# Kernel optimization log

Measured on AMD Instinct MI355X. Metric: run time of the kernel, lower is better.

Reference implementation:

```python
import jax, jax.numpy as jnp
import numpy as np

HIDDEN = 512
DETER = 1024
STOCH = 32
OBS = 1024
ACT = 64
B, T = 64, 256


def _linear_params(key, out_dim, in_dim):
    kw, kb = jax.random.split(key)
    scale = 1.0 / np.sqrt(in_dim)
    W = jax.random.uniform(kw, (out_dim, in_dim), jnp.float32, -scale, scale)
    b = jax.random.uniform(kb, (out_dim,), jnp.float32, -scale, scale)
    return W, b


def setup_inputs() -> dict:
    key = jax.random.key(0)
    ks = jax.random.split(key, 12)
    obs_embeds = jax.random.normal(ks[0], (B, T, OBS), jnp.float32)
    action_embs = jax.random.normal(ks[1], (B, T, ACT), jnp.float32)
    noise_prior = jax.random.normal(ks[2], (B, T, STOCH), jnp.float32)
    noise_post = jax.random.normal(ks[3], (B, T, STOCH), jnp.float32)
    W_sa, b_sa = _linear_params(ks[4], DETER, STOCH + ACT)
    W_ih, b_ih = _linear_params(ks[5], 3 * DETER, DETER)
    W_hh, b_hh = _linear_params(ks[6], 3 * DETER, DETER)
    Wp1, bp1 = _linear_params(ks[7], HIDDEN, DETER)
    Wp2, bp2 = _linear_params(ks[8], 2 * STOCH, HIDDEN)
    Wq1, bq1 = _linear_params(ks[9], HIDDEN, DETER + OBS)
    Wq2, bq2 = _linear_params(ks[10], 2 * STOCH, HIDDEN)
    return {
        "obs_embeds": obs_embeds, "action_embs": action_embs,
        "noise_prior": noise_prior, "noise_post": noise_post,
        "W_sa": W_sa, "b_sa": b_sa,
        "W_ih": W_ih, "b_ih": b_ih, "W_hh": W_hh, "b_hh": b_hh,
        "Wp1": Wp1, "bp1": bp1, "Wp2": Wp2, "bp2": bp2,
        "Wq1": Wq1, "bq1": bq1, "Wq2": Wq2, "bq2": bq2,
    }


def _rollout(obs_embeds, action_embs, noise_prior, noise_post,
             W_sa, b_sa, W_ih, b_ih, W_hh, b_hh,
             Wp1, bp1, Wp2, bp2, Wq1, bq1, Wq2, bq2):
    S = Wp2.shape[0] // 2
    eps = 1e-5

    def gru(x, h):  # torch GRUCell: gates ordered r, z, n
        gi = x @ W_ih.T + b_ih
        gh = h @ W_hh.T + b_hh
        ir, iz, inn = jnp.split(gi, 3, axis=-1)
        hr, hz, hn = jnp.split(gh, 3, axis=-1)
        r = jax.nn.sigmoid(ir + hr)
        z = jax.nn.sigmoid(iz + hz)
        n = jnp.tanh(inn + r * hn)
        return (1.0 - z) * n + z * h

    def step(carry, inp):
        deter, stoch = carry
        obs, act, n_p, n_q = inp
        # prior: h_t = f(s_{t-1}, a_{t-1}, h_{t-1})
        emb = jax.nn.relu(jnp.concatenate([stoch, act], -1) @ W_sa.T + b_sa)
        deter = gru(emb, deter)
        pm_s = jax.nn.relu(deter @ Wp1.T + bp1) @ Wp2.T + bp2
        p_mean = pm_s[..., :S]
        p_std = jax.nn.softplus(pm_s[..., S:]) + eps
        p_stoch = p_mean + p_std * n_p
        # posterior: p(s_t | h_t, o_t)
        qm_s = jax.nn.relu(jnp.concatenate([deter, obs], -1) @ Wq1.T + bq1) @ Wq2.T + bq2
        q_mean = qm_s[..., :S]
        q_std = jax.nn.softplus(qm_s[..., S:]) + eps
        q_stoch = q_mean + q_std * n_q
        out = jnp.concatenate([deter, p_mean, p_std, p_stoch, q_mean, q_std, q_stoch], -1)
        return (deter, q_stoch), out

    batch = obs_embeds.shape[0]
    deter0 = jnp.zeros((batch, W_hh.shape[1]), obs_embeds.dtype)
    stoch0 = jnp.zeros((batch, S), obs_embeds.dtype)
    xs = (
        jnp.swapaxes(obs_embeds, 0, 1),
        jnp.swapaxes(action_embs, 0, 1),
        jnp.swapaxes(noise_prior, 0, 1),
        jnp.swapaxes(noise_post, 0, 1),
    )
    _, outs = jax.lax.scan(step, (deter0, stoch0), xs)
    return jnp.swapaxes(outs, 0, 1)  # [B, T, deter + 6*stoch]


def reference(obs_embeds, action_embs, noise_prior, noise_post,
              W_sa, b_sa, W_ih, b_ih, W_hh, b_hh,
              Wp1, bp1, Wp2, bp2, Wq1, bq1, Wq2, bq2):
    return _rollout(obs_embeds, action_embs, noise_prior, noise_post,
                    W_sa, b_sa, W_ih, b_ih, W_hh, b_hh,
                    Wp1, bp1, Wp2, bp2, Wq1, bq1, Wq2, bq2)
```

## Files before the change

kernel.cpp:

```cpp
#include <hip/hip_runtime.h>
#include <math.h>

#define B_   64
#define T_   256
#define OUTD 1216

typedef unsigned short ushort_t;
typedef unsigned int   uint32;
typedef __attribute__((ext_vector_type(8))) short bfrag;
typedef __attribute__((ext_vector_type(4))) float f32x4;
typedef __attribute__((ext_vector_type(4))) unsigned short us4;

__device__ __forceinline__ float sigmoidf_(float x) { return 1.0f / (1.0f + __expf(-x)); }
__device__ __forceinline__ float softplusf_(float x) { return (x > 20.0f) ? x : log1pf(__expf(x)); }
__device__ __forceinline__ ushort_t f2bf(float f) {
    uint32 u = __float_as_uint(f);
    u += 0x7fffu + ((u >> 16) & 1u);
    return (ushort_t)(u >> 16);
}
__device__ __forceinline__ float bf2f(ushort_t u) { return __uint_as_float(((uint32)u) << 16); }

__global__ void kwprep(const float* __restrict__ Wih, const float* __restrict__ Whh,
                       const float* __restrict__ Wp1, const float* __restrict__ Wq1,
                       const float* __restrict__ Wp2, const float* __restrict__ Wq2,
                       const float* __restrict__ Wsa,
                       ushort_t* Wih_b, ushort_t* Whh_b, ushort_t* Wp1_b, ushort_t* Wq1_b,
                       ushort_t* W2sw, ushort_t* Wsasw) {
    int stride = gridDim.x * blockDim.x;
    int gid = blockIdx.x * blockDim.x + threadIdx.x;
    for (int i = gid; i < 3072 * 1024; i += stride) Wih_b[i] = f2bf(Wih[i]);
    for (int i = gid; i < 3072 * 1024; i += stride) Whh_b[i] = f2bf(Whh[i]);
    for (int i = gid; i < 512 * 1024; i += stride) Wp1_b[i] = f2bf(Wp1[i]);
    for (int i = gid; i < 512 * 2048; i += stride) Wq1_b[i] = f2bf(Wq1[i]);
    for (int i = gid; i < 65536; i += stride) {
        int head = i >> 15, g = (i >> 9) & 63, o = (i >> 3) & 63, ii = i & 7;
        const float* src = head ? Wq2 : Wp2;
        W2sw[i] = f2bf(src[o * 512 + g * 8 + ii]);
    }
    for (int i = gid; i < 98304; i += stride) {
        int g = i >> 13, j = (i >> 3) & 1023, ii = i & 7;
        Wsasw[i] = f2bf(Wsa[j * 96 + g * 8 + ii]);
    }
}

__global__ void kinit(const float* __restrict__ act, const float* __restrict__ Wsa,
                      const float* __restrict__ bsa,
                      ushort_t* emb_sw, ushort_t* det_sw0, float* det_fp0) {
    int gid = blockIdx.x * 256 + threadIdx.x;
    int j = gid >> 6, b = gid & 63;
    float acc = bsa[j];
    const float* a = act + (size_t)b * T_ * 64;
    const float* w = Wsa + j * 96 + 32;
#pragma unroll 8
    for (int c = 0; c < 64; ++c) acc += a[c] * w[c];
    emb_sw[((j >> 3) * 64 + b) * 8 + (j & 7)] = f2bf(fmaxf(acc, 0.f));
    det_sw0[gid] = 0;
    det_fp0[gid] = 0.f;
}

__global__ __launch_bounds__(256) void kgru(int t,
        const ushort_t* __restrict__ Wih, const ushort_t* __restrict__ Whh,
        const float* __restrict__ bih, const float* __restrict__ bhh,
        const ushort_t* __restrict__ emb_sw, const ushort_t* __restrict__ det_sw_in,
        const float* __restrict__ det_fp_in,
        ushort_t* __restrict__ det_sw_out, float* __restrict__ det_fp_out,
        const float* __restrict__ obs, ushort_t* __restrict__ obs_sw,
        float* __restrict__ out) {
    if (blockIdx.x >= 64) {
        int kb = (blockIdx.x - 64) * 64;
        int tx = threadIdx.x & 63, ty = threadIdx.x >> 6;
        for (int b = ty; b < 64; b += 4) {
            int k = kb + tx;
            float v = obs[((size_t)b * T_ + t) * 1024 + k];
            obs_sw[((k >> 3) * 64 + b) * 8 + (k & 7)] = f2bf(v);
        }
        return;
    }
    __shared__ float red[2 * 24 * 256];
    const int tid = threadIdx.x;
    const int lane = tid & 63, w = tid >> 6;
    const int m = lane & 15, quad = lane >> 4;
    const int j0 = blockIdx.x * 16;

    f32x4 acc[2][3][4];
#pragma unroll
    for (int a2 = 0; a2 < 2; ++a2)
#pragma unroll
        for (int g = 0; g < 3; ++g)
#pragma unroll
            for (int n = 0; n < 4; ++n) acc[a2][g][n] = (f32x4){0.f, 0.f, 0.f, 0.f};

    const int kb0 = w * 256;
    const ushort_t* arow[2][3];
#pragma unroll
    for (int g = 0; g < 3; ++g) {
        arow[0][g] = Wih + (size_t)(g * 1024 + j0 + m) * 1024 + kb0 + quad * 8;
        arow[1][g] = Whh + (size_t)(g * 1024 + j0 + m) * 1024 + kb0 + quad * 8;
    }
    const ushort_t* bx = emb_sw + ((kb0 >> 3) + quad) * 512 + m * 8;
    const ushort_t* bh = det_sw_in + ((kb0 >> 3) + quad) * 512 + m * 8;

#pragma unroll
    for (int it = 0; it < 8; ++it) {
        bfrag a[2][3], vx[4], vh[4];
#pragma unroll
        for (int g = 0; g < 3; ++g) {
            a[0][g] = *(const bfrag*)(arow[0][g] + it * 32);
            a[1][g] = *(const bfrag*)(arow[1][g] + it * 32);
        }
#pragma unroll
        for (int n = 0; n < 4; ++n) {
            vx[n] = *(const bfrag*)(bx + it * 2048 + n * 128);
            vh[n] = *(const bfrag*)(bh + it * 2048 + n * 128);
        }
#pragma unroll
        for (int g = 0; g < 3; ++g)
#pragma unroll
            for (int n = 0; n < 4; ++n) {
                acc[0][g][n] = __builtin_amdgcn_mfma_f32_16x16x32_bf16(a[0][g], vx[n], acc[0][g][n], 0, 0, 0);
                acc[1][g][n] = __builtin_amdgcn_mfma_f32_16x16x32_bf16(a[1][g], vh[n], acc[1][g][n], 0, 0, 0);
            }
    }

    if (w & 1) {
        float* dst = red + (w >> 1) * 6144;
#pragma unroll
        for (int a2 = 0; a2 < 2; ++a2)
#pragma unroll
            for (int g = 0; g < 3; ++g)
#pragma unroll
                for (int n = 0; n < 4; ++n)
                    *(f32x4*)(dst + ((a2 * 3 + g) * 4 + n) * 256 + lane * 4) = acc[a2][g][n];
    }
    __syncthreads();
    if (!(w & 1)) {
        float* dst = red + (w >> 1) * 6144;
#pragma unroll
        for (int a2 = 0; a2 < 2; ++a2)
#pragma unroll
            for (int g = 0; g < 3; ++g)
#pragma unroll
                for (int n = 0; n < 4; ++n) {
                    float* pp = dst + ((a2 * 3 + g) * 4 + n) * 256 + lane * 4;
                    f32x4 v = *(const f32x4*)pp;
                    v += acc[a2][g][n];
                    *(f32x4*)pp = v;
                }
    }
    __syncthreads();

    int b = tid >> 2, jq = tid & 3;
    int nt = b >> 4, bl = b & 15;
    int lsrc = (jq * 16 + bl) * 4;
    float gg[2][3][4];
#pragma unroll
    for (int a2 = 0; a2 < 2; ++a2)
#pragma unroll
        for (int g = 0; g < 3; ++g) {
            f32x4 v0 = *(const f32x4*)(red + ((a2 * 3 + g) * 4 + nt) * 256 + lsrc);
            f32x4 v1 = *(const f32x4*)(red + 6144 + ((a2 * 3 + g) * 4 + nt) * 256 + lsrc);
#pragma unroll
            for (int i = 0; i < 4; ++i) gg[a2][g][i] = v0[i] + v1[i];
        }
    f32x4 bi[3], bh2[3];
#pragma unroll
    for (int g = 0; g < 3; ++g) {
        bi[g] = *(const f32x4*)(bih + g * 1024 + j0 + jq * 4);
        bh2[g] = *(const f32x4*)(bhh + g * 1024 + j0 + jq * 4);
    }
    f32x4 h4;
    us4 dq;
#pragma unroll
    for (int i = 0; i < 4; ++i) {
        int j = j0 + jq * 4 + i;
        float r = sigmoidf_(gg[0][0][i] + bi[0][i] + gg[1][0][i] + bh2[0][i]);
        float z = sigmoidf_(gg[0][1][i] + bi[1][i] + gg[1][1][i] + bh2[1][i]);
        float n = tanhf(gg[0][2][i] + bi[2][i] + r * (gg[1][2][i] + bh2[2][i]));
        float hp = det_fp_in[j * 64 + b];
        float h = (1.f - z) * n + z * hp;
        h4[i] = h;
        dq[i] = f2bf(h);
        det_fp_out[j * 64 + b] = h;
    }
    *(f32x4*)(out + ((size_t)b * T_ + t) * OUTD + j0 + jq * 4) = h4;
    int kbase = j0 + jq * 4;
    *(us4*)(det_sw_out + ((kbase >> 3) * 64 + b) * 8 + (kbase & 7)) = dq;
}

__global__ __launch_bounds__(256) void khid(
        const ushort_t* __restrict__ Wp1b, const float* __restrict__ bp1,
        const ushort_t* __restrict__ Wq1b, const float* __restrict__ bq1,
        const ushort_t* __restrict__ det_sw, const ushort_t* __restrict__ obs_sw,
        float* __restrict__ pm1, float* __restrict__ qm1) {
    __shared__ float red[4 * 4 * 256];
    const int tid = threadIdx.x;
    const int lane = tid & 63, w = tid >> 6;
    const int m = lane & 15, quad = lane >> 4;
    const bool isq = blockIdx.x >= 32;
    const int j0 = (isq ? blockIdx.x - 32 : blockIdx.x) * 16;

    f32x4 acc[4];
#pragma unroll
    for (int n = 0; n < 4; ++n) acc[n] = (f32x4){0.f, 0.f, 0.f, 0.f};

    if (!isq) {
        const ushort_t* ar = Wp1b + (size_t)(j0 + m) * 1024 + w * 256 + quad * 8;
        const ushort_t* bb = det_sw + ((w * 32) + quad) * 512 + m * 8;
#pragma unroll
        for (int it = 0; it < 8; ++it) {
            bfrag a = *(const bfrag*)(ar + it * 32);
#pragma unroll
            for (int n = 0; n < 4; ++n) {
                bfrag v = *(const bfrag*)(bb + it * 2048 + n * 128);
                acc[n] = __builtin_amdgcn_mfma_f32_16x16x32_bf16(a, v, acc[n], 0, 0, 0);
            }
        }
    } else {
        int kb0 = w * 512;
        const ushort_t* bsrc = (w < 2) ? det_sw : obs_sw;
        int kloc = (w < 2) ? kb0 : kb0 - 1024;
        const ushort_t* ar = Wq1b + (size_t)(j0 + m) * 2048 + kb0 + quad * 8;
        const ushort_t* bb = bsrc + ((kloc >> 3) + quad) * 512 + m * 8;
#pragma unroll
        for (int it = 0; it < 16; ++it) {
            bfrag a = *(const bfrag*)(ar + it * 32);
#pragma unroll
            for (int n = 0; n < 4; ++n) {
                bfrag v = *(const bfrag*)(bb + it * 2048 + n * 128);
                acc[n] = __builtin_amdgcn_mfma_f32_16x16x32_bf16(a, v, acc[n], 0, 0, 0);
            }
        }
    }
#pragma unroll
    for (int n = 0; n < 4; ++n)
        *(f32x4*)(red + (w * 4 + n) * 256 + lane * 4) = acc[n];
    __syncthreads();

    int b = tid >> 2, jq = tid & 3;
    int nt = b >> 4, lsrc = (jq * 16 + (b & 15)) * 4;
    f32x4 s = (f32x4){0.f, 0.f, 0.f, 0.f};
#pragma unroll
    for (int w2 = 0; w2 < 4; ++w2) s += *(const f32x4*)(red + (w2 * 4 + nt) * 256 + lsrc);
    f32x4 bv = *(const f32x4*)((isq ? bq1 : bp1) + j0 + jq * 4);
    f32x4 r;
#pragma unroll
    for (int i = 0; i < 4; ++i) r[i] = fmaxf(s[i] + bv[i], 0.f);
    *(f32x4*)((isq ? qm1 : pm1) + (size_t)b * 512 + j0 + jq * 4) = r;
}

__global__ __launch_bounds__(256) void khead(int t,
        const float* __restrict__ pm1, const float* __restrict__ qm1,
        const float* __restrict__ bp2, const float* __restrict__ bq2,
        const ushort_t* __restrict__ W2sw, const ushort_t* __restrict__ Wsasw,
        const float* __restrict__ bsa,
        const float* __restrict__ n_p, const float* __restrict__ n_q,
        const float* __restrict__ act,
        float* __restrict__ out, ushort_t* __restrict__ emb_sw) {
    __shared__ float sh[1024 + 128 + 96];
    float* s_p = sh;
    float* s_q = sh + 512;
    float* s_head = sh + 1024;
    float* s_in = sh + 1152;
    const int b = blockIdx.x, tid = threadIdx.x;
    if (tid < 128) ((f32x4*)s_p)[tid] = ((const f32x4*)(pm1 + (size_t)b * 512))[tid];
    else ((f32x4*)s_q)[tid - 128] = ((const f32x4*)(qm1 + (size_t)b * 512))[tid - 128];
    if (t + 1 < T_ && tid < 64) s_in[32 + tid] = act[((size_t)b * T_ + t + 1) * 64 + tid];
    __syncthreads();
    if (tid < 128) {
        int head = tid >> 6, o = tid & 63;
        const ushort_t* wp = W2sw + head * 32768 + o * 8;
        const float* hv = head ? s_q : s_p;
        float acc2 = (head ? bq2 : bp2)[o];
#pragma unroll 4
        for (int g = 0; g < 64; ++g) {
            bfrag w8 = *(const bfrag*)(wp + g * 512);
#pragma unroll
            for (int i2 = 0; i2 < 8; ++i2) acc2 += hv[g * 8 + i2] * bf2f((ushort_t)w8[i2]);
        }
        s_head[tid] = acc2;
    }
    __syncthreads();
    if (tid < 64) {
        int s = tid & 31, isq = tid >> 5;
        float mean = s_head[isq * 64 + s];
        float raw = s_head[isq * 64 + 32 + s];
        float sd = softplusf_(raw) + 1e-5f;
        float noise = (isq ? n_q : n_p)[((size_t)b * T_ + t) * 32 + s];
        float st = mean + sd * noise;
        float* o = out + ((size_t)b * T_ + t) * OUTD + 1024 + isq * 96;
        o[s] = mean;
        o[32 + s] = sd;
        o[64 + s] = st;
        if (isq) s_in[s] = st;
    }
    __syncthreads();
    if (t + 1 < T_) {
#pragma unroll
        for (int q = 0; q < 4; ++q) {
            int j = q * 256 + tid;
            float acc2 = bsa[j];
#pragma unroll
            for (int g = 0; g < 12; ++g) {
                bfrag w8 = *(const bfrag*)(Wsasw + ((size_t)g * 1024 + j) * 8);
#pragma unroll
                for (int i2 = 0; i2 < 8; ++i2) acc2 += s_in[g * 8 + i2] * bf2f((ushort_t)w8[i2]);
            }
            emb_sw[((j >> 3) * 64 + b) * 8 + (j & 7)] = f2bf(fmaxf(acc2, 0.f));
        }
    }
}

extern "C" void kernel_launch(void* const* d_in, const int* in_sizes, int n_in,
                              void* d_out, int out_size, void* d_ws, size_t ws_size,
                              hipStream_t stream) {
    const float* obs = (const float*)d_in[0];
    const float* act = (const float*)d_in[1];
    const float* n_p = (const float*)d_in[2];
    const float* n_q = (const float*)d_in[3];
    const float* W_sa = (const float*)d_in[4];
    const float* b_sa = (const float*)d_in[5];
    const float* W_ih = (const float*)d_in[6];
    const float* b_ih = (const float*)d_in[7];
    const float* W_hh = (const float*)d_in[8];
    const float* b_hh = (const float*)d_in[9];
    const float* Wp1 = (const float*)d_in[10];
    const float* bp1 = (const float*)d_in[11];
    const float* Wp2 = (const float*)d_in[12];
    const float* bp2 = (const float*)d_in[13];
    const float* Wq1 = (const float*)d_in[14];
    const float* bq1 = (const float*)d_in[15];
    const float* Wq2 = (const float*)d_in[16];
    const float* bq2 = (const float*)d_in[17];
    float* out = (float*)d_out;

    char* p = (char*)d_ws;
    ushort_t* Wih_b = (ushort_t*)p;  p += (size_t)3145728 * 2;
    ushort_t* Whh_b = (ushort_t*)p;  p += (size_t)3145728 * 2;
    ushort_t* Wp1_b = (ushort_t*)p;  p += (size_t)524288 * 2;
    ushort_t* Wq1_b = (ushort_t*)p;  p += (size_t)1048576 * 2;
    ushort_t* W2sw  = (ushort_t*)p;  p += (size_t)65536 * 2;
    ushort_t* Wsasw = (ushort_t*)p;  p += (size_t)98304 * 2;
    ushort_t* emb_sw = (ushort_t*)p; p += (size_t)65536 * 2;
    ushort_t* obs_sw = (ushort_t*)p; p += (size_t)65536 * 2;
    ushort_t* det_sw0 = (ushort_t*)p; p += (size_t)65536 * 2;
    ushort_t* det_sw1 = (ushort_t*)p; p += (size_t)65536 * 2;
    float* det_fp0 = (float*)p; p += (size_t)65536 * 4;
    float* det_fp1 = (float*)p; p += (size_t)65536 * 4;
    float* pm1 = (float*)p; p += (size_t)32768 * 4;
    float* qm1 = (float*)p; p += (size_t)32768 * 4;

    kwprep<<<1024, 256, 0, stream>>>(W_ih, W_hh, Wp1, Wq1, Wp2, Wq2, W_sa,
                                     Wih_b, Whh_b, Wp1_b, Wq1_b, W2sw, Wsasw);
    kinit<<<256, 256, 0, stream>>>(act, W_sa, b_sa, emb_sw, det_sw0, det_fp0);

    for (int t = 0; t < T_; ++t) {
        ushort_t* dsw_in = (t & 1) ? det_sw1 : det_sw0;
        ushort_t* dsw_out = (t & 1) ? det_sw0 : det_sw1;
        float* dfp_in = (t & 1) ? det_fp1 : det_fp0;
        float* dfp_out = (t & 1) ? det_fp0 : det_fp1;
        kgru<<<80, 256, 0, stream>>>(t, Wih_b, Whh_b, b_ih, b_hh, emb_sw, dsw_in, dfp_in,
                                     dsw_out, dfp_out, obs, obs_sw, out);
        khid<<<64, 256, 0, stream>>>(Wp1_b, bp1, Wq1_b, bq1, dsw_out, obs_sw, pm1, qm1);
        khead<<<64, 256, 0, stream>>>(t, pm1, qm1, bp2, bq2, W2sw, Wsasw, b_sa,
                                      n_p, n_q, act, out, emb_sw);
    }
}
```

Baseline: 10.23 ms.

## Fuse per-timestep kernels into one persistent kernel with grid-wide atomic barriers

Replaces the 768 per-timestep launches (GRU, hidden MLP, head) with a single persistent 64-block kernel that loops over time and separates the stages with a global atomic-counter barrier. The obs bf16 conversion for step t+1 moves into the head stage, so the extra 16 conversion blocks are no longer needed. The aim is to remove kernel launch and teardown overhead on the serial recurrence. In exchange it relies on all 64 blocks being co-resident, and the spin barriers add their own latency.

```diff
diff --git a/kernel.cpp b/kernel.cpp
--- a/kernel.cpp
+++ b/kernel.cpp
@@ -4,6 +4,7 @@
 #define B_   64
 #define T_   256
 #define OUTD 1216
+#define NBLK 64
 
 typedef unsigned short ushort_t;
 typedef unsigned int   uint32;
@@ -25,9 +26,10 @@
                        const float* __restrict__ Wp2, const float* __restrict__ Wq2,
                        const float* __restrict__ Wsa,
                        ushort_t* Wih_b, ushort_t* Whh_b, ushort_t* Wp1_b, ushort_t* Wq1_b,
-                       ushort_t* W2sw, ushort_t* Wsasw) {
+                       ushort_t* W2sw, ushort_t* Wsasw, unsigned* barcnt) {
     int stride = gridDim.x * blockDim.x;
     int gid = blockIdx.x * blockDim.x + threadIdx.x;
+    if (gid == 0) *barcnt = 0u;
     for (int i = gid; i < 3072 * 1024; i += stride) Wih_b[i] = f2bf(Wih[i]);
     for (int i = gid; i < 3072 * 1024; i += stride) Whh_b[i] = f2bf(Whh[i]);
     for (int i = gid; i < 512 * 1024; i += stride) Wp1_b[i] = f2bf(Wp1[i]);
@@ -43,270 +45,295 @@
     }
 }
 
-__global__ void kinit(const float* __restrict__ act, const float* __restrict__ Wsa,
-                      const float* __restrict__ bsa,
-                      ushort_t* emb_sw, ushort_t* det_sw0, float* det_fp0) {
-    int gid = blockIdx.x * 256 + threadIdx.x;
-    int j = gid >> 6, b = gid & 63;
-    float acc = bsa[j];
-    const float* a = act + (size_t)b * T_ * 64;
-    const float* w = Wsa + j * 96 + 32;
-#pragma unroll 8
-    for (int c = 0; c < 64; ++c) acc += a[c] * w[c];
-    emb_sw[((j >> 3) * 64 + b) * 8 + (j & 7)] = f2bf(fmaxf(acc, 0.f));
-    det_sw0[gid] = 0;
-    det_fp0[gid] = 0.f;
-}
-
-__global__ __launch_bounds__(256) void kgru(int t,
+__device__ __forceinline__ void gbar(unsigned* cnt, unsigned& ep) {
+    __threadfence();
+    __syncthreads();
+    ++ep;
+    if (threadIdx.x == 0) {
+        __hip_atomic_fetch_add(cnt, 1u, __ATOMIC_RELEASE, __HIP_MEMORY_SCOPE_AGENT);
+        unsigned tgt = ep * (unsigned)NBLK;
+        while (__hip_atomic_load(cnt, __ATOMIC_ACQUIRE, __HIP_MEMORY_SCOPE_AGENT) < tgt)
+            __builtin_amdgcn_s_sleep(2);
+    }
+    __syncthreads();
+}
+
+__global__ __launch_bounds__(256, 1) void krssm(
+        const float* __restrict__ obs, const float* __restrict__ act,
+        const float* __restrict__ n_p, const float* __restrict__ n_q,
+        const float* __restrict__ Wsa, const float* __restrict__ bsa,
         const ushort_t* __restrict__ Wih, const ushort_t* __restrict__ Whh,
         const float* __restrict__ bih, const float* __restrict__ bhh,
-        const ushort_t* __restrict__ emb_sw, const ushort_t* __restrict__ det_sw_in,
-        const float* __restrict__ det_fp_in,
-        ushort_t* __restrict__ det_sw_out, float* __restrict__ det_fp_out,
-        const float* __restrict__ obs, ushort_t* __restrict__ obs_sw,
-        float* __restrict__ out) {
-    if (blockIdx.x >= 64) {
-        int kb = (blockIdx.x - 64) * 64;
-        int tx = threadIdx.x & 63, ty = threadIdx.x >> 6;
-        for (int b = ty; b < 64; b += 4) {
-            int k = kb + tx;
-            float v = obs[((size_t)b * T_ + t) * 1024 + k];
-            obs_sw[((k >> 3) * 64 + b) * 8 + (k & 7)] = f2bf(v);
-        }
-        return;
-    }
+        const ushort_t* __restrict__ Wp1b, const float* __restrict__ bp1,
+        const ushort_t* __restrict__ Wq1b, const float* __restrict__ bq1,
+        const ushort_t* __restrict__ W2sw, const ushort_t* __restrict__ Wsasw,
+        const float* __restrict__ bp2, const float* __restrict__ bq2,
+        ushort_t* emb_sw, ushort_t* obs_sw,
+        ushort_t* det_sw0, ushort_t* det_sw1, float* det_fp0, float* det_fp1,
+        float* pm1, float* qm1, float* out, unsigned* barcnt) {
     __shared__ float red[2 * 24 * 256];
     const int tid = threadIdx.x;
-    const int lane = tid & 63, w = tid >> 6;
-    const int m = lane & 15, quad = lane >> 4;
-    const int j0 = blockIdx.x * 16;
-
-    f32x4 acc[2][3][4];
-#pragma unroll
-    for (int a2 = 0; a2 < 2; ++a2)
-#pragma unroll
-        for (int g = 0; g < 3; ++g)
-#pragma unroll
-            for (int n = 0; n < 4; ++n) acc[a2][g][n] = (f32x4){0.f, 0.f, 0.f, 0.f};
-
-    const int kb0 = w * 256;
-    const ushort_t* arow[2][3];
-#pragma unroll
-    for (int g = 0; g < 3; ++g) {
-        arow[0][g] = Wih + (size_t)(g * 1024 + j0 + m) * 1024 + kb0 + quad * 8;
-        arow[1][g] = Whh + (size_t)(g * 1024 + j0 + m) * 1024 + kb0 + quad * 8;
-    }
-    const ushort_t* bx = emb_sw + ((kb0 >> 3) + quad) * 512 + m * 8;
-    const ushort_t* bh = det_sw_in + ((kb0 >> 3) + quad) * 512 + m * 8;
-
-#pragma unroll
-    for (int it = 0; it < 8; ++it) {
-        bfrag a[2][3], vx[4], vh[4];
-#pragma unroll
-        for (int g = 0; g < 3; ++g) {
-            a[0][g] = *(const bfrag*)(arow[0][g] + it * 32);
-            a[1][g] = *(const bfrag*)(arow[1][g] + it * 32);
+    const int blk = blockIdx.x;
+    unsigned ep = 0;
+
+    for (int idx = blk * 256 + tid; idx < 65536; idx += NBLK * 256) {
+        int j = idx >> 6, b = idx & 63;
+        float acc = bsa[j];
+        const float* a = act + (size_t)b * T_ * 64;
+        const float* w = Wsa + j * 96 + 32;
+#pragma unroll 8
+        for (int c = 0; c < 64; ++c) acc += a[c] * w[c];
+        emb_sw[((j >> 3) * 64 + b) * 8 + (j & 7)] = f2bf(fmaxf(acc, 0.f));
+        det_sw0[idx] = 0;
+        det_fp0[idx] = 0.f;
+    }
+    if (tid < 128) {
+        int g = tid;
+        const float* src = obs + (size_t)blk * T_ * 1024 + g * 8;
+        bfrag v;
+#pragma unroll
+        for (int i = 0; i < 8; ++i) v[i] = (short)f2bf(src[i]);
+        *(bfrag*)(obs_sw + ((size_t)g * 64 + blk) * 8) = v;
+    }
+    gbar(barcnt, ep);
+
+    ushort_t* dsw_in = det_sw0; ushort_t* dsw_out = det_sw1;
+    float* dfp_in = det_fp0;    float* dfp_out = det_fp1;
+
+#pragma unroll 1
+    for (int t = 0; t < T_; ++t) {
+        {
+            const int lane = tid & 63, w = tid >> 6;
+            const int m = lane & 15, quad = lane >> 4;
+            const int j0 = blk * 16;
+
+            f32x4 acc[2][3][4];
+#pragma unroll
+            for (int a2 = 0; a2 < 2; ++a2)
+#pragma unroll
+                for (int g = 0; g < 3; ++g)
+#pragma unroll
+                    for (int n = 0; n < 4; ++n) acc[a2][g][n] = (f32x4){0.f, 0.f, 0.f, 0.f};
+
+            const int kb0 = w * 256;
+            const ushort_t* arow[2][3];
+#pragma unroll
+            for (int g = 0; g < 3; ++g) {
+                arow[0][g] = Wih + (size_t)(g * 1024 + j0 + m) * 1024 + kb0 + quad * 8;
+                arow[1][g] = Whh + (size_t)(g * 1024 + j0 + m) * 1024 + kb0 + quad * 8;
+            }
+            const ushort_t* bx = emb_sw + ((kb0 >> 3) + quad) * 512 + m * 8;
+            const ushort_t* bh = dsw_in + ((kb0 >> 3) + quad) * 512 + m * 8;
+
+#pragma unroll
+            for (int it = 0; it < 8; ++it) {
+                bfrag a[2][3], vx[4], vh[4];
+#pragma unroll
+                for (int g = 0; g < 3; ++g) {
+                    a[0][g] = *(const bfrag*)(arow[0][g] + it * 32);
+                    a[1][g] = *(const bfrag*)(arow[1][g] + it * 32);
+                }
+#pragma unroll
+                for (int n = 0; n < 4; ++n) {
+                    vx[n] = *(const bfrag*)(bx + it * 2048 + n * 128);
+                    vh[n] = *(const bfrag*)(bh + it * 2048 + n * 128);
+                }
+#pragma unroll
+                for (int g = 0; g < 3; ++g)
+#pragma unroll
+                    for (int n = 0; n < 4; ++n) {
+                        acc[0][g][n] = __builtin_amdgcn_mfma_f32_16x16x32_bf16(a[0][g], vx[n], acc[0][g][n], 0, 0, 0);
+                        acc[1][g][n] = __builtin_amdgcn_mfma_f32_16x16x32_bf16(a[1][g], vh[n], acc[1][g][n], 0, 0, 0);
+                    }
+            }
+
+            if (w & 1) {
+                float* dst = red + (w >> 1) * 6144;
+#pragma unroll
+                for (int a2 = 0; a2 < 2; ++a2)
+#pragma unroll
+                    for (int g = 0; g < 3; ++g)
+#pragma unroll
+                        for (int n = 0; n < 4; ++n)
+                            *(f32x4*)(dst + ((a2 * 3 + g) * 4 + n) * 256 + lane * 4) = acc[a2][g][n];
+            }
+            __syncthreads();
+            if (!(w & 1)) {
+                float* dst = red + (w >> 1) * 6144;
+#pragma unroll
+                for (int a2 = 0; a2 < 2; ++a2)
+#pragma unroll
+                    for (int g = 0; g < 3; ++g)
+#pragma unroll
+                        for (int n = 0; n < 4; ++n) {
+                            float* pp = dst + ((a2 * 3 + g) * 4 + n) * 256 + lane * 4;
+                            f32x4 v = *(const f32x4*)pp;
+                            v += acc[a2][g][n];
+                            *(f32x4*)pp = v;
+                        }
+            }
+            __syncthreads();
+
+            int b = tid >> 2, jq = tid & 3;
+            int nt = b >> 4, bl = b & 15;
+            int lsrc = (jq * 16 + bl) * 4;
+            float gg[2][3][4];
+#pragma unroll
+            for (int a2 = 0; a2 < 2; ++a2)
+#pragma unroll
+                for (int g = 0; g < 3; ++g) {
+                    f32x4 v0 = *(const f32x4*)(red + ((a2 * 3 + g) * 4 + nt) * 256 + lsrc);
+                    f32x4 v1 = *(const f32x4*)(red + 6144 + ((a2 * 3 + g) * 4 + nt) * 256 + lsrc);
+#pragma unroll
+                    for (int i = 0; i < 4; ++i) gg[a2][g][i] = v0[i] + v1[i];
+                }
+            f32x4 bi[3], bh2[3];
+#pragma unroll
+            for (int g = 0; g < 3; ++g) {
+                bi[g] = *(const f32x4*)(bih + g * 1024 + j0 + jq * 4);
+                bh2[g] = *(const f32x4*)(bhh + g * 1024 + j0 + jq * 4);
+            }
+            f32x4 h4;
+            us4 dq;
+#pragma unroll
+            for (int i = 0; i < 4; ++i) {
+                int j = j0 + jq * 4 + i;
+                float r = sigmoidf_(gg[0][0][i] + bi[0][i] + gg[1][0][i] + bh2[0][i]);
+                float z = sigmoidf_(gg[0][1][i] + bi[1][i] + gg[1][1][i] + bh2[1][i]);
+                float n = tanhf(gg[0][2][i] + bi[2][i] + r * (gg[1][2][i] + bh2[2][i]));
+                float hp = dfp_in[j * 64 + b];
+                float h = (1.f - z) * n + z * hp;
+                h4[i] = h;
+                dq[i] = f2bf(h);
+                dfp_out[j * 64 + b] = h;
+            }
+            *(f32x4*)(out + ((size_t)b * T_ + t) * OUTD + j0 + jq * 4) = h4;
+            int kbase = j0 + jq * 4;
+            *(us4*)(dsw_out + ((kbase >> 3) * 64 + b) * 8 + (kbase & 7)) = dq;
         }
-#pragma unroll
-        for (int n = 0; n < 4; ++n) {
-            vx[n] = *(const bfrag*)(bx + it * 2048 + n * 128);
-            vh[n] = *(const bfrag*)(bh + it * 2048 + n * 128);
+        gbar(barcnt, ep);
+
+        {
+            const int lane = tid & 63, w = tid >> 6;
+            const int m = lane & 15, quad = lane >> 4;
+            const bool isq = blk >= 32;
+            const int j0 = (isq ? blk - 32 : blk) * 16;
+
+            f32x4 acc[4];
+#pragma unroll
+            for (int n = 0; n < 4; ++n) acc[n] = (f32x4){0.f, 0.f, 0.f, 0.f};
+
+            if (!isq) {
+                const ushort_t* ar = Wp1b + (size_t)(j0 + m) * 1024 + w * 256 + quad * 8;
+                const ushort_t* bb = dsw_out + ((w * 32) + quad) * 512 + m * 8;
+#pragma unroll
+                for (int it = 0; it < 8; ++it) {
+                    bfrag a = *(const bfrag*)(ar + it * 32);
+#pragma unroll
+                    for (int n = 0; n < 4; ++n) {
+                        bfrag v = *(const bfrag*)(bb + it * 2048 + n * 128);
+                        acc[n] = __builtin_amdgcn_mfma_f32_16x16x32_bf16(a, v, acc[n], 0, 0, 0);
+                    }
+                }
+            } else {
+                int kb0 = w * 512;
+                const ushort_t* bsrc = (w < 2) ? dsw_out : obs_sw;
+                int kloc = (w < 2) ? kb0 : kb0 - 1024;
+                const ushort_t* ar = Wq1b + (size_t)(j0 + m) * 2048 + kb0 + quad * 8;
+                const ushort_t* bb = bsrc + ((kloc >> 3) + quad) * 512 + m * 8;
+#pragma unroll
+                for (int it = 0; it < 16; ++it) {
+                    bfrag a = *(const bfrag*)(ar + it * 32);
+#pragma unroll
+                    for (int n = 0; n < 4; ++n) {
+                        bfrag v = *(const bfrag*)(bb + it * 2048 + n * 128);
+                        acc[n] = __builtin_amdgcn_mfma_f32_16x16x32_bf16(a, v, acc[n], 0, 0, 0);
+                    }
+                }
+            }
+#pragma unroll
+            for (int n = 0; n < 4; ++n)
+                *(f32x4*)(red + (w * 4 + n) * 256 + lane * 4) = acc[n];
+            __syncthreads();
+
+            int b = tid >> 2, jq = tid & 3;
+            int nt = b >> 4, lsrc = (jq * 16 + (b & 15)) * 4;
+            f32x4 s = (f32x4){0.f, 0.f, 0.f, 0.f};
+#pragma unroll
+            for (int w2 = 0; w2 < 4; ++w2) s += *(const f32x4*)(red + (w2 * 4 + nt) * 256 + lsrc);
+            f32x4 bv = *(const f32x4*)((isq ? bq1 : bp1) + j0 + jq * 4);
+            f32x4 r;
+#pragma unroll
+            for (int i = 0; i < 4; ++i) r[i] = fmaxf(s[i] + bv[i], 0.f);
+            *(f32x4*)((isq ? qm1 : pm1) + (size_t)b * 512 + j0 + jq * 4) = r;
         }
-#pragma unroll
-        for (int g = 0; g < 3; ++g)
-#pragma unroll
-            for (int n = 0; n < 4; ++n) {
-                acc[0][g][n] = __builtin_amdgcn_mfma_f32_16x16x32_bf16(a[0][g], vx[n], acc[0][g][n], 0, 0, 0);
-                acc[1][g][n] = __builtin_amdgcn_mfma_f32_16x16x32_bf16(a[1][g], vh[n], acc[1][g][n], 0, 0, 0);
-            }
-    }
-
-    if (w & 1) {
-        float* dst = red + (w >> 1) * 6144;
-#pragma unroll
-        for (int a2 = 0; a2 < 2; ++a2)
-#pragma unroll
-            for (int g = 0; g < 3; ++g)
-#pragma unroll
-                for (int n = 0; n < 4; ++n)
-                    *(f32x4*)(dst + ((a2 * 3 + g) * 4 + n) * 256 + lane * 4) = acc[a2][g][n];
-    }
-    __syncthreads();
-    if (!(w & 1)) {
-        float* dst = red + (w >> 1) * 6144;
-#pragma unroll
-        for (int a2 = 0; a2 < 2; ++a2)
-#pragma unroll
-            for (int g = 0; g < 3; ++g)
-#pragma unroll
-                for (int n = 0; n < 4; ++n) {
-                    float* pp = dst + ((a2 * 3 + g) * 4 + n) * 256 + lane * 4;
-                    f32x4 v = *(const f32x4*)pp;
-                    v += acc[a2][g][n];
-                    *(f32x4*)pp = v;
-                }
-    }
-    __syncthreads();
-
-    int b = tid >> 2, jq = tid & 3;
-    int nt = b >> 4, bl = b & 15;
-    int lsrc = (jq * 16 + bl) * 4;
-    float gg[2][3][4];
-#pragma unroll
-    for (int a2 = 0; a2 < 2; ++a2)
-#pragma unroll
-        for (int g = 0; g < 3; ++g) {
-            f32x4 v0 = *(const f32x4*)(red + ((a2 * 3 + g) * 4 + nt) * 256 + lsrc);
-            f32x4 v1 = *(const f32x4*)(red + 6144 + ((a2 * 3 + g) * 4 + nt) * 256 + lsrc);
-#pragma unroll
-            for (int i = 0; i < 4; ++i) gg[a2][g][i] = v0[i] + v1[i];
+        gbar(barcnt, ep);
+
+        {
+            float* s_p = red;
+            float* s_q = red + 512;
+            float* s_head = red + 1024;
+            float* s_in = red + 1152;
+            const int b = blk;
+            if (tid < 128) ((f32x4*)s_p)[tid] = ((const f32x4*)(pm1 + (size_t)b * 512))[tid];
+            else ((f32x4*)s_q)[tid - 128] = ((const f32x4*)(qm1 + (size_t)b * 512))[tid - 128];
+            if (t + 1 < T_ && tid < 64) s_in[32 + tid] = act[((size_t)b * T_ + t + 1) * 64 + tid];
+            if (t + 1 < T_ && tid >= 128) {
+                int g = tid - 128;
+                const float* src0 = obs + ((size_t)b * T_ + t + 1) * 1024 + g * 8;
+                bfrag v0;
+#pragma unroll
+                for (int i = 0; i < 8; ++i) v0[i] = (short)f2bf(src0[i]);
+                *(bfrag*)(obs_sw + ((size_t)g * 64 + b) * 8) = v0;
+            }
+            __syncthreads();
+            if (tid < 128) {
+                int head = tid >> 6, o = tid & 63;
+                const ushort_t* wp = W2sw + head * 32768 + o * 8;
+                const float* hv = head ? s_q : s_p;
+                float acc2 = (head ? bq2 : bp2)[o];
+#pragma unroll 4
+                for (int g = 0; g < 64; ++g) {
+                    bfrag w8 = *(const bfrag*)(wp + g * 512);
+#pragma unroll
+                    for (int i2 = 0; i2 < 8; ++i2) acc2 += hv[g * 8 + i2] * bf2f((ushort_t)w8[i2]);
+                }
+                s_head[tid] = acc2;
+            }
+            __syncthreads();
+            if (tid < 64) {
+                int s = tid & 31, isq = tid >> 5;
+                float mean = s_head[isq * 64 + s];
+                float raw = s_head[isq * 64 + 32 + s];
+                float sd = softplusf_(raw) + 1e-5f;
+                float noise = (isq ? n_q : n_p)[((size_t)b * T_ + t) * 32 + s];
+                float st = mean + sd * noise;
+                float* o = out + ((size_t)b * T_ + t) * OUTD + 1024 + isq * 96;
+                o[s] = mean;
+                o[32 + s] = sd;
+                o[64 + s] = st;
+                if (isq) s_in[s] = st;
+            }
+            __syncthreads();
+            if (t + 1 < T_) {
+#pragma unroll
+                for (int q = 0; q < 4; ++q) {
+                    int j = q * 256 + tid;
+                    float acc2 = bsa[j];
+#pragma unroll
+                    for (int g = 0; g < 12; ++g) {
+                        bfrag w8 = *(const bfrag*)(Wsasw + ((size_t)g * 1024 + j) * 8);
+#pragma unroll
+                        for (int i2 = 0; i2 < 8; ++i2) acc2 += s_in[g * 8 + i2] * bf2f((ushort_t)w8[i2]);
+                    }
+                    emb_sw[((j >> 3) * 64 + b) * 8 + (j & 7)] = f2bf(fmaxf(acc2, 0.f));
+                }
+            }
         }
-    f32x4 bi[3], bh2[3];
-#pragma unroll
-    for (int g = 0; g < 3; ++g) {
-        bi[g] = *(const f32x4*)(bih + g * 1024 + j0 + jq * 4);
-        bh2[g] = *(const f32x4*)(bhh + g * 1024 + j0 + jq * 4);
-    }
-    f32x4 h4;
-    us4 dq;
-#pragma unroll
-    for (int i = 0; i < 4; ++i) {
-        int j = j0 + jq * 4 + i;
-        float r = sigmoidf_(gg[0][0][i] + bi[0][i] + gg[1][0][i] + bh2[0][i]);
-        float z = sigmoidf_(gg[0][1][i] + bi[1][i] + gg[1][1][i] + bh2[1][i]);
-        float n = tanhf(gg[0][2][i] + bi[2][i] + r * (gg[1][2][i] + bh2[2][i]));
-        float hp = det_fp_in[j * 64 + b];
-        float h = (1.f - z) * n + z * hp;
-        h4[i] = h;
-        dq[i] = f2bf(h);
-        det_fp_out[j * 64 + b] = h;
-    }
-    *(f32x4*)(out + ((size_t)b * T_ + t) * OUTD + j0 + jq * 4) = h4;
-    int kbase = j0 + jq * 4;
-    *(us4*)(det_sw_out + ((kbase >> 3) * 64 + b) * 8 + (kbase & 7)) = dq;
-}
-
-__global__ __launch_bounds__(256) void khid(
-        const ushort_t* __restrict__ Wp1b, const float* __restrict__ bp1,
-        const ushort_t* __restrict__ Wq1b, const float* __restrict__ bq1,
-        const ushort_t* __restrict__ det_sw, const ushort_t* __restrict__ obs_sw,
-        float* __restrict__ pm1, float* __restrict__ qm1) {
-    __shared__ float red[4 * 4 * 256];
-    const int tid = threadIdx.x;
-    const int lane = tid & 63, w = tid >> 6;
-    const int m = lane & 15, quad = lane >> 4;
-    const bool isq = blockIdx.x >= 32;
-    const int j0 = (isq ? blockIdx.x - 32 : blockIdx.x) * 16;
-
-    f32x4 acc[4];
-#pragma unroll
-    for (int n = 0; n < 4; ++n) acc[n] = (f32x4){0.f, 0.f, 0.f, 0.f};
-
-    if (!isq) {
-        const ushort_t* ar = Wp1b + (size_t)(j0 + m) * 1024 + w * 256 + quad * 8;
-        const ushort_t* bb = det_sw + ((w * 32) + quad) * 512 + m * 8;
-#pragma unroll
-        for (int it = 0; it < 8; ++it) {
-            bfrag a = *(const bfrag*)(ar + it * 32);
-#pragma unroll
-            for (int n = 0; n < 4; ++n) {
-                bfrag v = *(const bfrag*)(bb + it * 2048 + n * 128);
-                acc[n] = __builtin_amdgcn_mfma_f32_16x16x32_bf16(a, v, acc[n], 0, 0, 0);
-            }
-        }
-    } else {
-        int kb0 = w * 512;
-        const ushort_t* bsrc = (w < 2) ? det_sw : obs_sw;
-        int kloc = (w < 2) ? kb0 : kb0 - 1024;
-        const ushort_t* ar = Wq1b + (size_t)(j0 + m) * 2048 + kb0 + quad * 8;
-        const ushort_t* bb = bsrc + ((kloc >> 3) + quad) * 512 + m * 8;
-#pragma unroll
-        for (int it = 0; it < 16; ++it) {
-            bfrag a = *(const bfrag*)(ar + it * 32);
-#pragma unroll
-            for (int n = 0; n < 4; ++n) {
-                bfrag v = *(const bfrag*)(bb + it * 2048 + n * 128);
-                acc[n] = __builtin_amdgcn_mfma_f32_16x16x32_bf16(a, v, acc[n], 0, 0, 0);
-            }
-        }
-    }
-#pragma unroll
-    for (int n = 0; n < 4; ++n)
-        *(f32x4*)(red + (w * 4 + n) * 256 + lane * 4) = acc[n];
-    __syncthreads();
-
-    int b = tid >> 2, jq = tid & 3;
-    int nt = b >> 4, lsrc = (jq * 16 + (b & 15)) * 4;
-    f32x4 s = (f32x4){0.f, 0.f, 0.f, 0.f};
-#pragma unroll
-    for (int w2 = 0; w2 < 4; ++w2) s += *(const f32x4*)(red + (w2 * 4 + nt) * 256 + lsrc);
-    f32x4 bv = *(const f32x4*)((isq ? bq1 : bp1) + j0 + jq * 4);
-    f32x4 r;
-#pragma unroll
-    for (int i = 0; i < 4; ++i) r[i] = fmaxf(s[i] + bv[i], 0.f);
-    *(f32x4*)((isq ? qm1 : pm1) + (size_t)b * 512 + j0 + jq * 4) = r;
-}
-
-__global__ __launch_bounds__(256) void khead(int t,
-        const float* __restrict__ pm1, const float* __restrict__ qm1,
-        const float* __restrict__ bp2, const float* __restrict__ bq2,
-        const ushort_t* __restrict__ W2sw, const ushort_t* __restrict__ Wsasw,
-        const float* __restrict__ bsa,
-        const float* __restrict__ n_p, const float* __restrict__ n_q,
-        const float* __restrict__ act,
-        float* __restrict__ out, ushort_t* __restrict__ emb_sw) {
-    __shared__ float sh[1024 + 128 + 96];
-    float* s_p = sh;
-    float* s_q = sh + 512;
-    float* s_head = sh + 1024;
-    float* s_in = sh + 1152;
-    const int b = blockIdx.x, tid = threadIdx.x;
-    if (tid < 128) ((f32x4*)s_p)[tid] = ((const f32x4*)(pm1 + (size_t)b * 512))[tid];
-    else ((f32x4*)s_q)[tid - 128] = ((const f32x4*)(qm1 + (size_t)b * 512))[tid - 128];
-    if (t + 1 < T_ && tid < 64) s_in[32 + tid] = act[((size_t)b * T_ + t + 1) * 64 + tid];
-    __syncthreads();
-    if (tid < 128) {
-        int head = tid >> 6, o = tid & 63;
-        const ushort_t* wp = W2sw + head * 32768 + o * 8;
-        const float* hv = head ? s_q : s_p;
-        float acc2 = (head ? bq2 : bp2)[o];
-#pragma unroll 4
-        for (int g = 0; g < 64; ++g) {
-            bfrag w8 = *(const bfrag*)(wp + g * 512);
-#pragma unroll
-            for (int i2 = 0; i2 < 8; ++i2) acc2 += hv[g * 8 + i2] * bf2f((ushort_t)w8[i2]);
-        }
-        s_head[tid] = acc2;
-    }
-    __syncthreads();
-    if (tid < 64) {
-        int s = tid & 31, isq = tid >> 5;
-        float mean = s_head[isq * 64 + s];
-        float raw = s_head[isq * 64 + 32 + s];
-        float sd = softplusf_(raw) + 1e-5f;
-        float noise = (isq ? n_q : n_p)[((size_t)b * T_ + t) * 32 + s];
-        float st = mean + sd * noise;
-        float* o = out + ((size_t)b * T_ + t) * OUTD + 1024 + isq * 96;
-        o[s] = mean;
-        o[32 + s] = sd;
-        o[64 + s] = st;
-        if (isq) s_in[s] = st;
-    }
-    __syncthreads();
-    if (t + 1 < T_) {
-#pragma unroll
-        for (int q = 0; q < 4; ++q) {
-            int j = q * 256 + tid;
-            float acc2 = bsa[j];
-#pragma unroll
-            for (int g = 0; g < 12; ++g) {
-                bfrag w8 = *(const bfrag*)(Wsasw + ((size_t)g * 1024 + j) * 8);
-#pragma unroll
-                for (int i2 = 0; i2 < 8; ++i2) acc2 += s_in[g * 8 + i2] * bf2f((ushort_t)w8[i2]);
-            }
-            emb_sw[((j >> 3) * 64 + b) * 8 + (j & 7)] = f2bf(fmaxf(acc2, 0.f));
-        }
+        gbar(barcnt, ep);
+
+        ushort_t* ts = dsw_in; dsw_in = dsw_out; dsw_out = ts;
+        float* tf = dfp_in; dfp_in = dfp_out; dfp_out = tf;
     }
 }
 
@@ -348,20 +375,14 @@
     float* det_fp1 = (float*)p; p += (size_t)65536 * 4;
     float* pm1 = (float*)p; p += (size_t)32768 * 4;
     float* qm1 = (float*)p; p += (size_t)32768 * 4;
+    unsigned* barcnt = (unsigned*)p; p += 256;
 
     kwprep<<<1024, 256, 0, stream>>>(W_ih, W_hh, Wp1, Wq1, Wp2, Wq2, W_sa,
-                                     Wih_b, Whh_b, Wp1_b, Wq1_b, W2sw, Wsasw);
-    kinit<<<256, 256, 0, stream>>>(act, W_sa, b_sa, emb_sw, det_sw0, det_fp0);
-
-    for (int t = 0; t < T_; ++t) {
-        ushort_t* dsw_in = (t & 1) ? det_sw1 : det_sw0;
-        ushort_t* dsw_out = (t & 1) ? det_sw0 : det_sw1;
-        float* dfp_in = (t & 1) ? det_fp1 : det_fp0;
-        float* dfp_out = (t & 1) ? det_fp0 : det_fp1;
-        kgru<<<80, 256, 0, stream>>>(t, Wih_b, Whh_b, b_ih, b_hh, emb_sw, dsw_in, dfp_in,
-                                     dsw_out, dfp_out, obs, obs_sw, out);
-        khid<<<64, 256, 0, stream>>>(Wp1_b, bp1, Wq1_b, bq1, dsw_out, obs_sw, pm1, qm1);
-        khead<<<64, 256, 0, stream>>>(t, pm1, qm1, bp2, bq2, W2sw, Wsasw, b_sa,
-                                      n_p, n_q, act, out, emb_sw);
-    }
-}
+                                     Wih_b, Whh_b, Wp1_b, Wq1_b, W2sw, Wsasw, barcnt);
+    krssm<<<NBLK, 256, 0, stream>>>(obs, act, n_p, n_q, W_sa, b_sa,
+                                    Wih_b, Whh_b, b_ih, b_hh,
+                                    Wp1_b, bp1, Wq1_b, bq1,
+                                    W2sw, Wsasw, bp2, bq2,
+                                    emb_sw, obs_sw, det_sw0, det_sw1,
+                                    det_fp0, det_fp1, pm1, qm1, out, barcnt);
+}
```

Result: slower. 23.22 ms (+126.9%).
